# Performance work log

Measured on AMD Instinct MI355X. Metric: run time of the kernel, lower is better.

Reference implementation:

```python
import jax, jax.numpy as jnp
import numpy as np

NODE_DIM = 256
OUT_DIM = 512
NUM_HEADS = 8
HEAD_DIM = 32
HID = NUM_HEADS * HEAD_DIM  # 256
N_NODES = 200000
N_GRAPHS = 2000


def _linear_init(key, fan_in, fan_out):
    lim = 1.0 / np.sqrt(fan_in)
    kw, kb = jax.random.split(key)
    w = jax.random.uniform(kw, (fan_in, fan_out), minval=-lim, maxval=lim, dtype=jnp.float32)
    b = jax.random.uniform(kb, (fan_out,), minval=-lim, maxval=lim, dtype=jnp.float32)
    return w, b


def setup_inputs() -> dict:
    key = jax.random.key(0)
    ks = jax.random.split(key, 16)
    inp = {}
    inp["node_embeddings"] = jax.random.normal(ks[0], (N_NODES, NODE_DIM), dtype=jnp.float32)
    inp["node_to_graph_id"] = jnp.sort(jax.random.randint(ks[1], (N_NODES,), 0, N_GRAPHS)).astype(jnp.int64)
    inp["num_graphs"] = N_GRAPHS
    # weighted_mean pooler params
    inp["wm_score_w1"], inp["wm_score_b1"] = _linear_init(ks[2], NODE_DIM, HID)
    inp["wm_score_w2"], inp["wm_score_b2"] = _linear_init(ks[3], HID, NUM_HEADS)
    inp["wm_val_w1"], inp["wm_val_b1"] = _linear_init(ks[4], NODE_DIM, HID)
    inp["wm_val_w2"], inp["wm_val_b2"] = _linear_init(ks[5], HID, NUM_HEADS * HEAD_DIM)
    inp["wm_comb_w"] = _linear_init(ks[6], NUM_HEADS * HEAD_DIM, OUT_DIM)[0]
    # weighted_sum pooler params
    inp["ws_score_w1"], inp["ws_score_b1"] = _linear_init(ks[7], NODE_DIM, HID)
    inp["ws_score_w2"], inp["ws_score_b2"] = _linear_init(ks[8], HID, NUM_HEADS)
    inp["ws_val_w1"], inp["ws_val_b1"] = _linear_init(ks[9], NODE_DIM, HID)
    inp["ws_val_w2"], inp["ws_val_b2"] = _linear_init(ks[10], HID, NUM_HEADS * HEAD_DIM)
    inp["ws_comb_w"] = _linear_init(ks[11], NUM_HEADS * HEAD_DIM, OUT_DIM)[0]
    # max pooler + final combination
    inp["mx_comb_w"] = _linear_init(ks[12], NODE_DIM, OUT_DIM)[0]
    inp["final_w"] = _linear_init(ks[13], 3 * OUT_DIM, OUT_DIM)[0]
    return inp


def _mlp(x, w1, b1, w2, b2):
    return jax.nn.relu(x @ w1 + b1) @ w2 + b2


def _scatter_softmax(scores, seg, num_graphs):
    # scores: [N, H]; softmax over nodes within each graph, per head
    m = jax.ops.segment_max(scores, seg, num_segments=num_graphs)
    m = jnp.where(jnp.isfinite(m), m, 0.0)  # empty graphs
    e = jnp.exp(scores - m[seg])
    s = jax.ops.segment_sum(e, seg, num_segments=num_graphs)
    return e / s[seg]


def _multihead_readout(x, seg, num_graphs, sw1, sb1, sw2, sb2, vw1, vb1, vw2, vb2, cw, weighted_mean):
    scores = _mlp(x, sw1, sb1, sw2, sb2)                       # [N, heads]
    if weighted_mean:
        weights = _scatter_softmax(scores, seg, num_graphs)
    else:
        weights = jax.nn.sigmoid(scores)
    values = _mlp(x, vw1, vb1, vw2, vb2).reshape(-1, NUM_HEADS, HEAD_DIM)
    weighted = (weights[:, :, None] * values).reshape(-1, NUM_HEADS * HEAD_DIM)
    per_graph = jax.ops.segment_sum(weighted, seg, num_segments=num_graphs)
    return per_graph @ cw


def reference(node_embeddings, node_to_graph_id, num_graphs,
              wm_score_w1, wm_score_b1, wm_score_w2, wm_score_b2,
              wm_val_w1, wm_val_b1, wm_val_w2, wm_val_b2, wm_comb_w,
              ws_score_w1, ws_score_b1, ws_score_w2, ws_score_b2,
              ws_val_w1, ws_val_b1, ws_val_w2, ws_val_b2, ws_comb_w,
              mx_comb_w, final_w):
    seg = node_to_graph_id.astype(jnp.int32)
    mean_repr = _multihead_readout(node_embeddings, seg, num_graphs,
                                   wm_score_w1, wm_score_b1, wm_score_w2, wm_score_b2,
                                   wm_val_w1, wm_val_b1, wm_val_w2, wm_val_b2, wm_comb_w, True)
    sum_repr = _multihead_readout(node_embeddings, seg, num_graphs,
                                  ws_score_w1, ws_score_b1, ws_score_w2, ws_score_b2,
                                  ws_val_w1, ws_val_b1, ws_val_w2, ws_val_b2, ws_comb_w, False)
    pg_max = jax.ops.segment_max(node_embeddings, seg, num_segments=num_graphs)
    pg_max = jnp.where(jnp.isfinite(pg_max), pg_max, 0.0)  # torch_scatter zeros empty segments
    max_repr = pg_max @ mx_comb_w
    raw = jnp.concatenate([mean_repr, sum_repr, max_repr], axis=1)  # [G, 3*out_dim]
    return jax.nn.relu(raw) @ final_w
```

## Files before the change

### kernel.cpp

```cpp
#include <hip/hip_runtime.h>
#include <hip/hip_bf16.h>

typedef __bf16 bf16_t;
typedef __bf16 bf16x8 __attribute__((ext_vector_type(8)));
typedef float  f32x4  __attribute__((ext_vector_type(4)));

#define MFMA16(a, b, c) __builtin_amdgcn_mfma_f32_16x16x32_bf16((a), (b), (c), 0, 0, 0)

#define ROWS 48

__device__ __forceinline__ int gray(int row) { return (row ^ (row >> 1)) & 7; }
__device__ __forceinline__ int swz256(int row, int col) {
    return row * 256 + ((((col >> 3) ^ gray(row)) << 3) | (col & 7));
}

__device__ __forceinline__ bf16x8 cvt8(float4 a, float4 b) {
    bf16x8 o;
    o[0] = (bf16_t)a.x; o[1] = (bf16_t)a.y; o[2] = (bf16_t)a.z; o[3] = (bf16_t)a.w;
    o[4] = (bf16_t)b.x; o[5] = (bf16_t)b.y; o[6] = (bf16_t)b.z; o[7] = (bf16_t)b.w;
    return o;
}

__device__ __forceinline__ unsigned enc_max(float x) {
    unsigned b = __float_as_uint(x);
    return (b & 0x80000000u) ? ~b : (b | 0x80000000u);
}
__device__ __forceinline__ float dec_max(unsigned e) {
    if (e == 0u) return 0.0f;
    return (e & 0x80000000u) ? __uint_as_float(e ^ 0x80000000u) : __uint_as_float(~e);
}

__device__ __forceinline__ void gemm256p(const bf16_t* __restrict__ As,
                                         const bf16_t* __restrict__ Wk,
                                         f32x4 acc[3][2], int w, int l) {
    const int l15 = l & 15, hi = l >> 4;
#pragma unroll
    for (int mt = 0; mt < 3; ++mt)
#pragma unroll
        for (int j = 0; j < 2; ++j) acc[mt][j] = (f32x4){0.f, 0.f, 0.f, 0.f};

    const bf16_t* wb = Wk + ((size_t)hi * 256 + w * 32 + l15) * 8;

    bf16x8 b0[3], b1[3];
    bf16x8 a[2][3];
    b0[0] = *(const bf16x8*)(wb);
    b1[0] = *(const bf16x8*)(wb + 128);
    b0[1] = *(const bf16x8*)(wb + 8192);
    b1[1] = *(const bf16x8*)(wb + 8192 + 128);
#pragma unroll
    for (int mt = 0; mt < 3; ++mt) {
        const int row = mt * 16 + l15;
        a[0][mt] = *(const bf16x8*)(As + row * 256 + (hi ^ gray(row)) * 8);
    }

#pragma unroll
    for (int kt = 0; kt < 8; ++kt) {
        const int cur = kt % 3, nx2 = (kt + 2) % 3;
        if (kt + 2 < 8) {
            b0[nx2] = *(const bf16x8*)(wb + (kt + 2) * 8192);
            b1[nx2] = *(const bf16x8*)(wb + (kt + 2) * 8192 + 128);
        }
        if (kt + 1 < 8) {
#pragma unroll
            for (int mt = 0; mt < 3; ++mt) {
                const int row = mt * 16 + l15;
                a[(kt + 1) & 1][mt] =
                    *(const bf16x8*)(As + row * 256 + (((kt + 1) * 4 + hi) ^ gray(row)) * 8);
            }
        }
#pragma unroll
        for (int mt = 0; mt < 3; ++mt) {
            acc[mt][0] = MFMA16(a[kt & 1][mt], b0[cur], acc[mt][0]);
            acc[mt][1] = MFMA16(a[kt & 1][mt], b1[cur], acc[mt][1]);
        }
    }
}

__device__ __forceinline__ void write_h(f32x4 acc[3][2], const float* __restrict__ bias,
                                        bool relu, bf16_t* __restrict__ dst, int w, int l) {
    const int l15 = l & 15, hi = l >> 4;
#pragma unroll
    for (int j = 0; j < 2; ++j) {
        const int col = w * 32 + j * 16 + l15;
        const float bv = bias[col];
#pragma unroll
        for (int mt = 0; mt < 3; ++mt)
#pragma unroll
            for (int r = 0; r < 4; ++r) {
                const int row = mt * 16 + hi * 4 + r;
                float v = acc[mt][j][r] + bv;
                if (relu) v = fmaxf(v, 0.f);
                dst[swz256(row, col)] = (bf16_t)v;
            }
    }
}

__device__ __forceinline__ void gemm_score(const bf16_t* __restrict__ As,
                                           const bf16_t* __restrict__ W2k,
                                           const float* __restrict__ b2,
                                           float* __restrict__ ssc, int coloff, int w, int l) {
    if (w >= 3) return;
    const int l15 = l & 15, hi = l >> 4;
    const int row = w * 16 + l15;
    const bf16_t* wb = W2k + ((size_t)hi * 16 + l15) * 8;
    bf16x8 b[3];
    b[0] = *(const bf16x8*)(wb);
    b[1] = *(const bf16x8*)(wb + 512);
    f32x4 acc = (f32x4){0.f, 0.f, 0.f, 0.f};
#pragma unroll
    for (int kt = 0; kt < 8; ++kt) {
        const int cur = kt % 3, nx2 = (kt + 2) % 3;
        if (kt + 2 < 8) b[nx2] = *(const bf16x8*)(wb + (kt + 2) * 512);
        bf16x8 a = *(const bf16x8*)(As + row * 256 + ((kt * 4 + hi) ^ gray(row)) * 8);
        acc = MFMA16(a, b[cur], acc);
    }
    if (l15 < 8) {
        const float bv = b2[l15];
#pragma unroll
        for (int r = 0; r < 4; ++r) {
            const int orow = w * 16 + hi * 4 + r;
            ssc[orow * 16 + coloff + l15] = acc[r] + bv;
        }
    }
}

template <bool WM>
__device__ __forceinline__ void reduce_seg(const bf16_t* __restrict__ sh,
                                           const float* __restrict__ ssc,
                                           const bf16_t* __restrict__ sx,
                                           const int* __restrict__ sseg,
                                           float* __restrict__ num, float* __restrict__ den,
                                           unsigned* __restrict__ pmax, int G) {
    const int col = threadIdx.x & 255;
    const int rbeg = (threadIdx.x >> 8) * 24;
    float av = 0.f, ad = 0.f;
    unsigned am = 0u;
    int gcur = sseg[rbeg];
    for (int r = rbeg; r < rbeg + 24; ++r) {
        const int g = sseg[r];
        if (g != gcur) {
            if ((unsigned)gcur < (unsigned)G) {
                atomicAdd(&num[(size_t)gcur * 256 + col], av);
                if (WM) {
                    if (col < 8) atomicAdd(&den[(size_t)gcur * 8 + col], ad);
                    atomicMax(&pmax[(size_t)gcur * 256 + col], am);
                }
            }
            av = 0.f; ad = 0.f; am = 0u; gcur = g;
        }
        const int si = swz256(r, col);
        const float v = (float)sh[si];
        const float wgt = ssc[r * 16 + (WM ? 0 : 8) + (col >> 5)];
        av += wgt * v;
        if (WM) {
            if (col < 8) ad += ssc[r * 16 + col];
            am = max(am, enc_max((float)sx[si]));
        }
    }
    if ((unsigned)gcur < (unsigned)G) {
        atomicAdd(&num[(size_t)gcur * 256 + col], av);
        if (WM) {
            if (col < 8) atomicAdd(&den[(size_t)gcur * 8 + col], ad);
            atomicMax(&pmax[(size_t)gcur * 256 + col], am);
        }
    }
}

__global__ __launch_bounds__(512, 3) void node_kernel(
    const float* __restrict__ X, const int* __restrict__ seg,
    const bf16_t* __restrict__ wt_sw1_wm, const bf16_t* __restrict__ wt_sw2_wm,
    const bf16_t* __restrict__ wt_vw1_wm, const bf16_t* __restrict__ wt_vw2_wm,
    const bf16_t* __restrict__ wt_sw1_ws, const bf16_t* __restrict__ wt_sw2_ws,
    const bf16_t* __restrict__ wt_vw1_ws, const bf16_t* __restrict__ wt_vw2_ws,
    const float* __restrict__ b_sw1_wm, const float* __restrict__ b_sw2_wm,
    const float* __restrict__ b_vw1_wm, const float* __restrict__ b_vw2_wm,
    const float* __restrict__ b_sw1_ws, const float* __restrict__ b_sw2_ws,
    const float* __restrict__ b_vw1_ws, const float* __restrict__ b_vw2_ws,
    float* __restrict__ num_wm, float* __restrict__ den_wm,
    float* __restrict__ acc_ws, unsigned* __restrict__ pmax, int N, int G) {
    __shared__ __align__(16) bf16_t sx[ROWS * 256];
    __shared__ __align__(16) bf16_t sh[ROWS * 256];
    __shared__ float ssc[ROWS * 16];
    __shared__ int sseg[ROWS];

    const int tid = threadIdx.x;
    const int w = tid >> 6, l = tid & 63;
    const int r0 = blockIdx.x * ROWS;

#pragma unroll
    for (int i = 0; i < 3; ++i) {
        const int cid = tid + i * 512;
        const int row = cid >> 5, ch = cid & 31;
        bf16x8 o;
        if (r0 + row < N) {
            const float4* gp = (const float4*)(X + (size_t)(r0 + row) * 256 + ch * 8);
            o = cvt8(gp[0], gp[1]);
        } else {
            for (int j = 0; j < 8; ++j) o[j] = (bf16_t)0.f;
        }
        *(bf16x8*)(sx + row * 256 + (ch ^ gray(row)) * 8) = o;
    }
    if (tid < ROWS) sseg[tid] = (r0 + tid < N) ? seg[r0 + tid] : -1;
    __syncthreads();

    f32x4 acc[3][2];

    gemm256p(sx, wt_sw1_wm, acc, w, l);
    write_h(acc, b_sw1_wm, true, sh, w, l);
    __syncthreads();
    gemm_score(sh, wt_sw2_wm, b_sw2_wm, ssc, 0, w, l);
    __syncthreads();

    gemm256p(sx, wt_sw1_ws, acc, w, l);
    write_h(acc, b_sw1_ws, true, sh, w, l);
    __syncthreads();
    gemm_score(sh, wt_sw2_ws, b_sw2_ws, ssc, 8, w, l);
    __syncthreads();

#pragma unroll
    for (int i = 0; i < 2; ++i) {
        const int idx = tid + i * 512;
        if (idx < ROWS * 16) {
            const float v = ssc[idx];
            ssc[idx] = ((idx & 15) < 8) ? __expf(v) : 1.f / (1.f + __expf(-v));
        }
    }
    __syncthreads();

    gemm256p(sx, wt_vw1_wm, acc, w, l);
    write_h(acc, b_vw1_wm, true, sh, w, l);
    __syncthreads();
    gemm256p(sh, wt_vw2_wm, acc, w, l);
    __syncthreads();
    write_h(acc, b_vw2_wm, false, sh, w, l);
    __syncthreads();
    reduce_seg<true>(sh, ssc, sx, sseg, num_wm, den_wm, pmax, G);
    __syncthreads();

    gemm256p(sx, wt_vw1_ws, acc, w, l);
    write_h(acc, b_vw1_ws, true, sh, w, l);
    __syncthreads();
    gemm256p(sh, wt_vw2_ws, acc, w, l);
    __syncthreads();
    write_h(acc, b_vw2_ws, false, sx, w, l);
    __syncthreads();
    reduce_seg<false>(sx, ssc, sx, sseg, acc_ws, nullptr, nullptr, G);
}

__global__ __launch_bounds__(256, 2) void graph_kernel(
    const float* __restrict__ num_wm, const float* __restrict__ den_wm,
    const float* __restrict__ acc_ws, const unsigned* __restrict__ pmax,
    const bf16_t* __restrict__ wt_comb_wm, const bf16_t* __restrict__ wt_comb_ws,
    const bf16_t* __restrict__ wt_comb_mx, const bf16_t* __restrict__ wt_final,
    float* __restrict__ out, int G) {
    __shared__ __align__(16) bf16_t sa[16 * 256];
    __shared__ __align__(16) bf16_t sraw[16 * 1536];

    const int tid = threadIdx.x, w = tid >> 6, l = tid & 63;
    const int l15 = l & 15, hi = l >> 4;
    const int g0 = blockIdx.x * 16;

    for (int src = 0; src < 3; ++src) {
#pragma unroll
        for (int i = 0; i < 2; ++i) {
            const int cid = tid + i * 256;
            const int row = cid >> 5, ch = cid & 31;
            const int g = g0 + row;
            bf16x8 o;
            if (g < G) {
                if (src == 0) {
                    const float4* np = (const float4*)(num_wm + (size_t)g * 256 + ch * 8);
                    float4 v0 = np[0], v1 = np[1];
                    const float d = den_wm[(size_t)g * 8 + (ch >> 2)];
                    const float rd = (d > 0.f) ? 1.f / d : 0.f;
                    o[0] = (bf16_t)(v0.x * rd); o[1] = (bf16_t)(v0.y * rd);
                    o[2] = (bf16_t)(v0.z * rd); o[3] = (bf16_t)(v0.w * rd);
                    o[4] = (bf16_t)(v1.x * rd); o[5] = (bf16_t)(v1.y * rd);
                    o[6] = (bf16_t)(v1.z * rd); o[7] = (bf16_t)(v1.w * rd);
                } else if (src == 1) {
                    const float4* np = (const float4*)(acc_ws + (size_t)g * 256 + ch * 8);
                    o = cvt8(np[0], np[1]);
                } else {
                    const unsigned* mp = pmax + (size_t)g * 256 + ch * 8;
#pragma unroll
                    for (int j = 0; j < 8; ++j) o[j] = (bf16_t)dec_max(mp[j]);
                }
            } else {
                for (int j = 0; j < 8; ++j) o[j] = (bf16_t)0.f;
            }
            *(bf16x8*)(sa + row * 256 + (ch ^ gray(row)) * 8) = o;
        }
        __syncthreads();

        const bf16_t* Wt = (src == 0) ? wt_comb_wm : ((src == 1) ? wt_comb_ws : wt_comb_mx);
        bf16x8 a[8];
#pragma unroll
        for (int kt = 0; kt < 8; ++kt)
            a[kt] = *(const bf16x8*)(sa + l15 * 256 + ((kt * 4 + hi) ^ gray(l15)) * 8);
        f32x4 acc[8];
#pragma unroll
        for (int j = 0; j < 8; ++j) acc[j] = (f32x4){0.f, 0.f, 0.f, 0.f};
#pragma unroll
        for (int kt = 0; kt < 8; ++kt) {
            bf16x8 b[8];
#pragma unroll
            for (int j = 0; j < 8; ++j) {
                const int ncol = (w * 8 + j) * 16 + l15;
                b[j] = *(const bf16x8*)(Wt + ((size_t)(kt * 4 + hi) * 512 + ncol) * 8);
            }
#pragma unroll
            for (int j = 0; j < 8; ++j) acc[j] = MFMA16(a[kt], b[j], acc[j]);
        }
#pragma unroll
        for (int j = 0; j < 8; ++j) {
            const int col = src * 512 + (w * 8 + j) * 16 + l15;
#pragma unroll
            for (int r = 0; r < 4; ++r) {
                const int row = hi * 4 + r;
                const float v = fmaxf(acc[j][r], 0.f);
                sraw[row * 1536 + ((((col >> 3) ^ gray(row)) << 3) | (col & 7))] = (bf16_t)v;
            }
        }
        __syncthreads();
    }

    f32x4 facc[8];
#pragma unroll
    for (int j = 0; j < 8; ++j) facc[j] = (f32x4){0.f, 0.f, 0.f, 0.f};
    for (int kt = 0; kt < 48; ++kt) {
        bf16x8 a = *(const bf16x8*)(sraw + l15 * 1536 + ((kt * 4 + hi) ^ gray(l15)) * 8);
#pragma unroll
        for (int j = 0; j < 8; ++j) {
            const int ncol = (w * 8 + j) * 16 + l15;
            bf16x8 b = *(const bf16x8*)(wt_final + ((size_t)(kt * 4 + hi) * 512 + ncol) * 8);
            facc[j] = MFMA16(a, b, facc[j]);
        }
    }
#pragma unroll
    for (int j = 0; j < 8; ++j) {
        const int col = (w * 8 + j) * 16 + l15;
#pragma unroll
        for (int r = 0; r < 4; ++r) {
            const int row = hi * 4 + r;
            if (g0 + row < G) out[(size_t)(g0 + row) * 512 + col] = facc[j][r];
        }
    }
}

struct PrepTab {
    const float* src[12];
    bf16_t* dst[12];
    int K[12], Nn[12], Nout[12];
    int base[13];
};

__global__ void prep_all(PrepTab t) {
    const int idx = blockIdx.x * blockDim.x + threadIdx.x;
    if (idx >= t.base[12]) return;
    int i = 0;
#pragma unroll
    for (int s = 0; s < 12; ++s)
        if (idx >= t.base[s + 1]) i = s + 1;
    const int local = idx - t.base[i];
    const int j = local & 7;
    const int rest = local >> 3;
    const int n = rest % t.Nout[i];
    const int kc = rest / t.Nout[i];
    const int k = kc * 8 + j;
    const float v = (n < t.Nn[i]) ? t.src[i][(size_t)k * t.Nn[i] + n] : 0.f;
    t.dst[i][local] = (bf16_t)v;
}

extern "C" void kernel_launch(void* const* d_in, const int* in_sizes, int n_in,
                              void* d_out, int out_size, void* d_ws, size_t ws_size,
                              hipStream_t stream) {
    const float* X = (const float*)d_in[0];
    const int* seg = (const int*)d_in[1];
    const int N = in_sizes[1];
    const int G = out_size / 512;

    float* num_wm = (float*)d_ws;
    float* acc_ws = num_wm + (size_t)G * 256;
    float* den_wm = acc_ws + (size_t)G * 256;
    unsigned* pmax = (unsigned*)(den_wm + (size_t)G * 8);
    bf16_t* wt = (bf16_t*)(pmax + (size_t)G * 256);

    bf16_t* wt_sw1_wm = wt;
    bf16_t* wt_sw2_wm = wt_sw1_wm + 65536;
    bf16_t* wt_vw1_wm = wt_sw2_wm + 4096;
    bf16_t* wt_vw2_wm = wt_vw1_wm + 65536;
    bf16_t* wt_sw1_ws = wt_vw2_wm + 65536;
    bf16_t* wt_sw2_ws = wt_sw1_ws + 65536;
    bf16_t* wt_vw1_ws = wt_sw2_ws + 4096;
    bf16_t* wt_vw2_ws = wt_vw1_ws + 65536;
    bf16_t* wt_comb_wm = wt_vw2_ws + 65536;
    bf16_t* wt_comb_ws = wt_comb_wm + 131072;
    bf16_t* wt_comb_mx = wt_comb_ws + 131072;
    bf16_t* wt_final = wt_comb_mx + 131072;

    const size_t accum_bytes = ((size_t)G * 256 * 3 + (size_t)G * 8) * 4;
    hipMemsetAsync(d_ws, 0, accum_bytes, stream);

    struct TT { int srcIdx; bf16_t* dst; int K, Nn, Nout; };
    const TT tt[12] = {
        {3,  wt_sw1_wm, 256, 256, 256},  {5,  wt_sw2_wm, 256, 8,   16},
        {7,  wt_vw1_wm, 256, 256, 256},  {9,  wt_vw2_wm, 256, 256, 256},
        {12, wt_sw1_ws, 256, 256, 256},  {14, wt_sw2_ws, 256, 8,   16},
        {16, wt_vw1_ws, 256, 256, 256},  {18, wt_vw2_ws, 256, 256, 256},
        {11, wt_comb_wm, 256, 512, 512}, {20, wt_comb_ws, 256, 512, 512},
        {21, wt_comb_mx, 256, 512, 512}, {22, wt_final, 1536, 512, 512},
    };
    PrepTab pt;
    int base = 0;
    for (int i = 0; i < 12; ++i) {
        pt.src[i] = (const float*)d_in[tt[i].srcIdx];
        pt.dst[i] = tt[i].dst;
        pt.K[i] = tt[i].K; pt.Nn[i] = tt[i].Nn; pt.Nout[i] = tt[i].Nout;
        pt.base[i] = base;
        base += tt[i].K * tt[i].Nout;
    }
    pt.base[12] = base;
    prep_all<<<(base + 255) / 256, 256, 0, stream>>>(pt);

    const int nb = (N + ROWS - 1) / ROWS;
    node_kernel<<<nb, 512, 0, stream>>>(
        X, seg,
        wt_sw1_wm, wt_sw2_wm, wt_vw1_wm, wt_vw2_wm,
        wt_sw1_ws, wt_sw2_ws, wt_vw1_ws, wt_vw2_ws,
        (const float*)d_in[4], (const float*)d_in[6], (const float*)d_in[8], (const float*)d_in[10],
        (const float*)d_in[13], (const float*)d_in[15], (const float*)d_in[17], (const float*)d_in[19],
        num_wm, den_wm, acc_ws, pmax, N, G);

    const int gb = (G + 15) / 16;
    graph_kernel<<<gb, 256, 0, stream>>>(num_wm, den_wm, acc_ws, pmax,
                                         wt_comb_wm, wt_comb_ws, wt_comb_mx, wt_final,
                                         (float*)d_out, G);
}
```

Baseline: 302.9 us.

## Vectorize segment reductions and split sum/max work across thread halves

Replaces the per-column scalar segment reduction with an 8-wide bf16x8 vectorized version, where each thread owns 8 columns over 6 rows. The weighted-sum and max reductions now run concurrently on separate halves of the block instead of one thread doing both. The denominator is accumulated with one atomic per row and head rather than per segment run. This is meant to cut LDS load instructions and serial loop length in the reduction phase, at the cost of more global atomics, since runs are split over 6-row chunks, and idle threads in the second reduction.

```diff
diff --git a/kernel.cpp b/kernel.cpp
--- a/kernel.cpp
+++ b/kernel.cpp
@@ -125,44 +125,70 @@
 }
 
 template <bool WM>
-__device__ __forceinline__ void reduce_seg(const bf16_t* __restrict__ sh,
-                                           const float* __restrict__ ssc,
-                                           const bf16_t* __restrict__ sx,
-                                           const int* __restrict__ sseg,
-                                           float* __restrict__ num, float* __restrict__ den,
-                                           unsigned* __restrict__ pmax, int G) {
-    const int col = threadIdx.x & 255;
-    const int rbeg = (threadIdx.x >> 8) * 24;
-    float av = 0.f, ad = 0.f;
-    unsigned am = 0u;
+__device__ __forceinline__ void reduce_sum_vec(const bf16_t* __restrict__ sh,
+                                               const float* __restrict__ ssc,
+                                               const int* __restrict__ sseg,
+                                               float* __restrict__ num, int G, int tid) {
+    const int cg = tid & 31;
+    const int rbeg = (tid >> 5) * 6;
+    const int off = (WM ? 0 : 8) + (cg >> 2);
+    float s[8];
+#pragma unroll
+    for (int j = 0; j < 8; ++j) s[j] = 0.f;
     int gcur = sseg[rbeg];
-    for (int r = rbeg; r < rbeg + 24; ++r) {
+    for (int r = rbeg; r < rbeg + 6; ++r) {
         const int g = sseg[r];
         if (g != gcur) {
             if ((unsigned)gcur < (unsigned)G) {
-                atomicAdd(&num[(size_t)gcur * 256 + col], av);
-                if (WM) {
-                    if (col < 8) atomicAdd(&den[(size_t)gcur * 8 + col], ad);
-                    atomicMax(&pmax[(size_t)gcur * 256 + col], am);
-                }
-            }
-            av = 0.f; ad = 0.f; am = 0u; gcur = g;
-        }
-        const int si = swz256(r, col);
-        const float v = (float)sh[si];
-        const float wgt = ssc[r * 16 + (WM ? 0 : 8) + (col >> 5)];
-        av += wgt * v;
-        if (WM) {
-            if (col < 8) ad += ssc[r * 16 + col];
-            am = max(am, enc_max((float)sx[si]));
-        }
+#pragma unroll
+                for (int j = 0; j < 8; ++j)
+                    atomicAdd(&num[(size_t)gcur * 256 + cg * 8 + j], s[j]);
+            }
+#pragma unroll
+            for (int j = 0; j < 8; ++j) s[j] = 0.f;
+            gcur = g;
+        }
+        const float wgt = ssc[r * 16 + off];
+        const bf16x8 v = *(const bf16x8*)(sh + r * 256 + (cg ^ gray(r)) * 8);
+#pragma unroll
+        for (int j = 0; j < 8; ++j) s[j] += wgt * (float)v[j];
     }
     if ((unsigned)gcur < (unsigned)G) {
-        atomicAdd(&num[(size_t)gcur * 256 + col], av);
-        if (WM) {
-            if (col < 8) atomicAdd(&den[(size_t)gcur * 8 + col], ad);
-            atomicMax(&pmax[(size_t)gcur * 256 + col], am);
-        }
+#pragma unroll
+        for (int j = 0; j < 8; ++j)
+            atomicAdd(&num[(size_t)gcur * 256 + cg * 8 + j], s[j]);
+    }
+}
+
+__device__ __forceinline__ void max_vec(const bf16_t* __restrict__ sx,
+                                        const int* __restrict__ sseg,
+                                        unsigned* __restrict__ pmax, int G, int tid2) {
+    const int cg = tid2 & 31;
+    const int rbeg = (tid2 >> 5) * 6;
+    unsigned am[8];
+#pragma unroll
+    for (int j = 0; j < 8; ++j) am[j] = 0u;
+    int gcur = sseg[rbeg];
+    for (int r = rbeg; r < rbeg + 6; ++r) {
+        const int g = sseg[r];
+        if (g != gcur) {
+            if ((unsigned)gcur < (unsigned)G) {
+#pragma unroll
+                for (int j = 0; j < 8; ++j)
+                    atomicMax(&pmax[(size_t)gcur * 256 + cg * 8 + j], am[j]);
+            }
+#pragma unroll
+            for (int j = 0; j < 8; ++j) am[j] = 0u;
+            gcur = g;
+        }
+        const bf16x8 v = *(const bf16x8*)(sx + r * 256 + (cg ^ gray(r)) * 8);
+#pragma unroll
+        for (int j = 0; j < 8; ++j) am[j] = max(am[j], enc_max((float)v[j]));
+    }
+    if ((unsigned)gcur < (unsigned)G) {
+#pragma unroll
+        for (int j = 0; j < 8; ++j)
+            atomicMax(&pmax[(size_t)gcur * 256 + cg * 8 + j], am[j]);
     }
 }
 
@@ -234,7 +260,16 @@
     __syncthreads();
     write_h(acc, b_vw2_wm, false, sh, w, l);
     __syncthreads();
-    reduce_seg<true>(sh, ssc, sx, sseg, num_wm, den_wm, pmax, G);
+    if (tid < 256)
+        reduce_sum_vec<true>(sh, ssc, sseg, num_wm, G, tid);
+    else
+        max_vec(sx, sseg, pmax, G, tid - 256);
+    if (tid < ROWS * 8) {
+        const int row = tid >> 3, h = tid & 7;
+        const int g = sseg[row];
+        if ((unsigned)g < (unsigned)G)
+            atomicAdd(&den_wm[(size_t)g * 8 + h], ssc[row * 16 + h]);
+    }
     __syncthreads();
 
     gemm256p(sx, wt_vw1_ws, acc, w, l);
@@ -244,7 +279,8 @@
     __syncthreads();
     write_h(acc, b_vw2_ws, false, sx, w, l);
     __syncthreads();
-    reduce_seg<false>(sx, ssc, sx, sseg, acc_ws, nullptr, nullptr, G);
+    if (tid < 256)
+        reduce_sum_vec<false>(sx, ssc, sseg, acc_ws, G, tid);
 }
 
 __global__ __launch_bounds__(256, 2) void graph_kernel(
```

New measurement: 957.3 us. 3.16x slower.

## Pair the two poolers' first-layer GEMMs to share A-tile loads and cut barriers

Applied to the files above, without the earlier changes.

Adds a paired GEMM that computes the weighted-mean and weighted-sum first-layer projections together, so each A fragment read from shared memory feeds both weight sets. The two score heads now run at the same time on different wave groups. A second hidden buffer keeps both intermediate activations resident, which lets several barriers go. The launch bound is raised from 3 to 4 blocks per CU. The cost is more shared memory per block (an extra 24KB) and double the accumulator registers in the paired GEMM, so the higher occupancy target may not be met or may force register spills.

```diff
diff --git a/kernel.cpp b/kernel.cpp
--- a/kernel.cpp
+++ b/kernel.cpp
@@ -28,6 +28,58 @@
 __device__ __forceinline__ float dec_max(unsigned e) {
     if (e == 0u) return 0.0f;
     return (e & 0x80000000u) ? __uint_as_float(e ^ 0x80000000u) : __uint_as_float(~e);
+}
+
+__device__ __forceinline__ void gemm256_pair(const bf16_t* __restrict__ As,
+                                             const bf16_t* __restrict__ WkA,
+                                             const bf16_t* __restrict__ WkB,
+                                             f32x4 accA[3][2], f32x4 accB[3][2],
+                                             int w, int l) {
+    const int l15 = l & 15, hi = l >> 4;
+#pragma unroll
+    for (int mt = 0; mt < 3; ++mt)
+#pragma unroll
+        for (int j = 0; j < 2; ++j) {
+            accA[mt][j] = (f32x4){0.f, 0.f, 0.f, 0.f};
+            accB[mt][j] = (f32x4){0.f, 0.f, 0.f, 0.f};
+        }
+    const bf16_t* wbA = WkA + ((size_t)hi * 256 + w * 32 + l15) * 8;
+    const bf16_t* wbB = WkB + ((size_t)hi * 256 + w * 32 + l15) * 8;
+
+    bf16x8 bA0[2], bA1[2], bB0[2], bB1[2];
+    bf16x8 a[2][3];
+    bA0[0] = *(const bf16x8*)(wbA);
+    bA1[0] = *(const bf16x8*)(wbA + 128);
+    bB0[0] = *(const bf16x8*)(wbB);
+    bB1[0] = *(const bf16x8*)(wbB + 128);
+#pragma unroll
+    for (int mt = 0; mt < 3; ++mt) {
+        const int row = mt * 16 + l15;
+        a[0][mt] = *(const bf16x8*)(As + row * 256 + (hi ^ gray(row)) * 8);
+    }
+#pragma unroll
+    for (int kt = 0; kt < 8; ++kt) {
+        const int cur = kt & 1, nxt = cur ^ 1;
+        if (kt + 1 < 8) {
+            bA0[nxt] = *(const bf16x8*)(wbA + (kt + 1) * 8192);
+            bA1[nxt] = *(const bf16x8*)(wbA + (kt + 1) * 8192 + 128);
+            bB0[nxt] = *(const bf16x8*)(wbB + (kt + 1) * 8192);
+            bB1[nxt] = *(const bf16x8*)(wbB + (kt + 1) * 8192 + 128);
+#pragma unroll
+            for (int mt = 0; mt < 3; ++mt) {
+                const int row = mt * 16 + l15;
+                a[nxt][mt] =
+                    *(const bf16x8*)(As + row * 256 + (((kt + 1) * 4 + hi) ^ gray(row)) * 8);
+            }
+        }
+#pragma unroll
+        for (int mt = 0; mt < 3; ++mt) {
+            accA[mt][0] = MFMA16(a[cur][mt], bA0[cur], accA[mt][0]);
+            accA[mt][1] = MFMA16(a[cur][mt], bA1[cur], accA[mt][1]);
+            accB[mt][0] = MFMA16(a[cur][mt], bB0[cur], accB[mt][0]);
+            accB[mt][1] = MFMA16(a[cur][mt], bB1[cur], accB[mt][1]);
+        }
+    }
 }
 
 __device__ __forceinline__ void gemm256p(const bf16_t* __restrict__ As,
@@ -98,10 +150,9 @@
 __device__ __forceinline__ void gemm_score(const bf16_t* __restrict__ As,
                                            const bf16_t* __restrict__ W2k,
                                            const float* __restrict__ b2,
-                                           float* __restrict__ ssc, int coloff, int w, int l) {
-    if (w >= 3) return;
+                                           float* __restrict__ ssc, int coloff, int rt, int l) {
     const int l15 = l & 15, hi = l >> 4;
-    const int row = w * 16 + l15;
+    const int row = rt * 16 + l15;
     const bf16_t* wb = W2k + ((size_t)hi * 16 + l15) * 8;
     bf16x8 b[3];
     b[0] = *(const bf16x8*)(wb);
@@ -118,7 +169,7 @@
         const float bv = b2[l15];
 #pragma unroll
         for (int r = 0; r < 4; ++r) {
-            const int orow = w * 16 + hi * 4 + r;
+            const int orow = rt * 16 + hi * 4 + r;
             ssc[orow * 16 + coloff + l15] = acc[r] + bv;
         }
     }
@@ -166,7 +217,7 @@
     }
 }
 
-__global__ __launch_bounds__(512, 3) void node_kernel(
+__global__ __launch_bounds__(512, 4) void node_kernel(
     const float* __restrict__ X, const int* __restrict__ seg,
     const bf16_t* __restrict__ wt_sw1_wm, const bf16_t* __restrict__ wt_sw2_wm,
     const bf16_t* __restrict__ wt_vw1_wm, const bf16_t* __restrict__ wt_vw2_wm,
@@ -179,7 +230,8 @@
     float* __restrict__ num_wm, float* __restrict__ den_wm,
     float* __restrict__ acc_ws, unsigned* __restrict__ pmax, int N, int G) {
     __shared__ __align__(16) bf16_t sx[ROWS * 256];
-    __shared__ __align__(16) bf16_t sh[ROWS * 256];
+    __shared__ __align__(16) bf16_t shm[ROWS * 256];
+    __shared__ __align__(16) bf16_t shs[ROWS * 256];
     __shared__ float ssc[ROWS * 16];
     __shared__ int sseg[ROWS];
 
@@ -203,18 +255,17 @@
     if (tid < ROWS) sseg[tid] = (r0 + tid < N) ? seg[r0 + tid] : -1;
     __syncthreads();
 
-    f32x4 acc[3][2];
-
-    gemm256p(sx, wt_sw1_wm, acc, w, l);
-    write_h(acc, b_sw1_wm, true, sh, w, l);
-    __syncthreads();
-    gemm_score(sh, wt_sw2_wm, b_sw2_wm, ssc, 0, w, l);
-    __syncthreads();
-
-    gemm256p(sx, wt_sw1_ws, acc, w, l);
-    write_h(acc, b_sw1_ws, true, sh, w, l);
-    __syncthreads();
-    gemm_score(sh, wt_sw2_ws, b_sw2_ws, ssc, 8, w, l);
+    f32x4 accA[3][2], accB[3][2];
+
+    gemm256_pair(sx, wt_sw1_wm, wt_sw1_ws, accA, accB, w, l);
+    write_h(accA, b_sw1_wm, true, shm, w, l);
+    write_h(accB, b_sw1_ws, true, shs, w, l);
+    __syncthreads();
+
+    if (w < 3)
+        gemm_score(shm, wt_sw2_wm, b_sw2_wm, ssc, 0, w, l);
+    else if (w >= 4 && w < 7)
+        gemm_score(shs, wt_sw2_ws, b_sw2_ws, ssc, 8, w - 4, l);
     __syncthreads();
 
 #pragma unroll
@@ -227,24 +278,22 @@
     }
     __syncthreads();
 
-    gemm256p(sx, wt_vw1_wm, acc, w, l);
-    write_h(acc, b_vw1_wm, true, sh, w, l);
-    __syncthreads();
-    gemm256p(sh, wt_vw2_wm, acc, w, l);
-    __syncthreads();
-    write_h(acc, b_vw2_wm, false, sh, w, l);
-    __syncthreads();
-    reduce_seg<true>(sh, ssc, sx, sseg, num_wm, den_wm, pmax, G);
-    __syncthreads();
-
-    gemm256p(sx, wt_vw1_ws, acc, w, l);
-    write_h(acc, b_vw1_ws, true, sh, w, l);
-    __syncthreads();
-    gemm256p(sh, wt_vw2_ws, acc, w, l);
-    __syncthreads();
-    write_h(acc, b_vw2_ws, false, sx, w, l);
-    __syncthreads();
-    reduce_seg<false>(sx, ssc, sx, sseg, acc_ws, nullptr, nullptr, G);
+    gemm256_pair(sx, wt_vw1_wm, wt_vw1_ws, accA, accB, w, l);
+    write_h(accA, b_vw1_wm, true, shm, w, l);
+    write_h(accB, b_vw1_ws, true, shs, w, l);
+    __syncthreads();
+
+    gemm256p(shm, wt_vw2_wm, accA, w, l);
+    __syncthreads();
+    write_h(accA, b_vw2_wm, false, shm, w, l);
+    __syncthreads();
+    reduce_seg<true>(shm, ssc, sx, sseg, num_wm, den_wm, pmax, G);
+
+    gemm256p(shs, wt_vw2_ws, accA, w, l);
+    __syncthreads();
+    write_h(accA, b_vw2_ws, false, shs, w, l);
+    __syncthreads();
+    reduce_seg<false>(shs, ssc, sx, sseg, acc_ws, nullptr, nullptr, G);
 }
 
 __global__ __launch_bounds__(256, 2) void graph_kernel(
```

Result: slower. 354.9 us (+17.2%).

## Split node kernel across two grid rows, one per pooler

Applied to the files above, without the earlier changes.

The node kernel now launches a 2D grid where blockIdx.y picks either the weighted-mean or the weighted-sum pooler. Each block computes only one score MLP and one value MLP, halving the serial per-block work and doubling the block count. The max-pool reduction moves to the weighted-sum half. The cost is that every block reloads and converts its 48-row X tile, doubling input reads from global memory, and shared score storage is halved.

```diff
diff --git a/kernel.cpp b/kernel.cpp
--- a/kernel.cpp
+++ b/kernel.cpp
@@ -98,7 +98,7 @@
 __device__ __forceinline__ void gemm_score(const bf16_t* __restrict__ As,
                                            const bf16_t* __restrict__ W2k,
                                            const float* __restrict__ b2,
-                                           float* __restrict__ ssc, int coloff, int w, int l) {
+                                           float* __restrict__ ssc, int w, int l) {
     if (w >= 3) return;
     const int l15 = l & 15, hi = l >> 4;
     const int row = w * 16 + l15;
@@ -119,7 +119,7 @@
 #pragma unroll
         for (int r = 0; r < 4; ++r) {
             const int orow = w * 16 + hi * 4 + r;
-            ssc[orow * 16 + coloff + l15] = acc[r] + bv;
+            ssc[orow * 8 + l15] = acc[r] + bv;
         }
     }
 }
@@ -143,6 +143,7 @@
                 atomicAdd(&num[(size_t)gcur * 256 + col], av);
                 if (WM) {
                     if (col < 8) atomicAdd(&den[(size_t)gcur * 8 + col], ad);
+                } else {
                     atomicMax(&pmax[(size_t)gcur * 256 + col], am);
                 }
             }
@@ -150,10 +151,11 @@
         }
         const int si = swz256(r, col);
         const float v = (float)sh[si];
-        const float wgt = ssc[r * 16 + (WM ? 0 : 8) + (col >> 5)];
+        const float wgt = ssc[r * 8 + (col >> 5)];
         av += wgt * v;
         if (WM) {
-            if (col < 8) ad += ssc[r * 16 + col];
+            if (col < 8) ad += ssc[r * 8 + col];
+        } else {
             am = max(am, enc_max((float)sx[si]));
         }
     }
@@ -161,6 +163,7 @@
         atomicAdd(&num[(size_t)gcur * 256 + col], av);
         if (WM) {
             if (col < 8) atomicAdd(&den[(size_t)gcur * 8 + col], ad);
+        } else {
             atomicMax(&pmax[(size_t)gcur * 256 + col], am);
         }
     }
@@ -180,12 +183,22 @@
     float* __restrict__ acc_ws, unsigned* __restrict__ pmax, int N, int G) {
     __shared__ __align__(16) bf16_t sx[ROWS * 256];
     __shared__ __align__(16) bf16_t sh[ROWS * 256];
-    __shared__ float ssc[ROWS * 16];
+    __shared__ float ssc[ROWS * 8];
     __shared__ int sseg[ROWS];
 
     const int tid = threadIdx.x;
     const int w = tid >> 6, l = tid & 63;
     const int r0 = blockIdx.x * ROWS;
+    const bool wm = (blockIdx.y == 0);
+
+    const bf16_t* Ws1 = wm ? wt_sw1_wm : wt_sw1_ws;
+    const bf16_t* Ws2 = wm ? wt_sw2_wm : wt_sw2_ws;
+    const bf16_t* Wv1 = wm ? wt_vw1_wm : wt_vw1_ws;
+    const bf16_t* Wv2 = wm ? wt_vw2_wm : wt_vw2_ws;
+    const float* bs1 = wm ? b_sw1_wm : b_sw1_ws;
+    const float* bs2 = wm ? b_sw2_wm : b_sw2_ws;
+    const float* bv1 = wm ? b_vw1_wm : b_vw1_ws;
+    const float* bv2 = wm ? b_vw2_wm : b_vw2_ws;
 
 #pragma unroll
     for (int i = 0; i < 3; ++i) {
@@ -205,46 +218,30 @@
 
     f32x4 acc[3][2];
 
-    gemm256p(sx, wt_sw1_wm, acc, w, l);
-    write_h(acc, b_sw1_wm, true, sh, w, l);
-    __syncthreads();
-    gemm_score(sh, wt_sw2_wm, b_sw2_wm, ssc, 0, w, l);
-    __syncthreads();
-
-    gemm256p(sx, wt_sw1_ws, acc, w, l);
-    write_h(acc, b_sw1_ws, true, sh, w, l);
-    __syncthreads();
-    gemm_score(sh, wt_sw2_ws, b_sw2_ws, ssc, 8, w, l);
-    __syncthreads();
-
-#pragma unroll
-    for (int i = 0; i < 2; ++i) {
-        const int idx = tid + i * 512;
-        if (idx < ROWS * 16) {
-            const float v = ssc[idx];
-            ssc[idx] = ((idx & 15) < 8) ? __expf(v) : 1.f / (1.f + __expf(-v));
-        }
-    }
-    __syncthreads();
-
-    gemm256p(sx, wt_vw1_wm, acc, w, l);
-    write_h(acc, b_vw1_wm, true, sh, w, l);
-    __syncthreads();
-    gemm256p(sh, wt_vw2_wm, acc, w, l);
-    __syncthreads();
-    write_h(acc, b_vw2_wm, false, sh, w, l);
-    __syncthreads();
-    reduce_seg<true>(sh, ssc, sx, sseg, num_wm, den_wm, pmax, G);
-    __syncthreads();
-
-    gemm256p(sx, wt_vw1_ws, acc, w, l);
-    write_h(acc, b_vw1_ws, true, sh, w, l);
-    __syncthreads();
-    gemm256p(sh, wt_vw2_ws, acc, w, l);
-    __syncthreads();
-    write_h(acc, b_vw2_ws, false, sx, w, l);
-    __syncthreads();
-    reduce_seg<false>(sx, ssc, sx, sseg, acc_ws, nullptr, nullptr, G);
+    gemm256p(sx, Ws1, acc, w, l);
+    write_h(acc, bs1, true, sh, w, l);
+    __syncthreads();
+    gemm_score(sh, Ws2, bs2, ssc, w, l);
+    __syncthreads();
+
+    if (tid < ROWS * 8) {
+        const float v = ssc[tid];
+        ssc[tid] = wm ? __expf(v) : 1.f / (1.f + __expf(-v));
+    }
+    __syncthreads();
+
+    gemm256p(sx, Wv1, acc, w, l);
+    write_h(acc, bv1, true, sh, w, l);
+    __syncthreads();
+    gemm256p(sh, Wv2, acc, w, l);
+    __syncthreads();
+    write_h(acc, bv2, false, sh, w, l);
+    __syncthreads();
+
+    if (wm)
+        reduce_seg<true>(sh, ssc, sx, sseg, num_wm, den_wm, nullptr, G);
+    else
+        reduce_seg<false>(sh, ssc, sx, sseg, acc_ws, nullptr, pmax, G);
 }
 
 __global__ __launch_bounds__(256, 2) void graph_kernel(
@@ -423,7 +420,8 @@
     prep_all<<<(base + 255) / 256, 256, 0, stream>>>(pt);
 
     const int nb = (N + ROWS - 1) / ROWS;
-    node_kernel<<<nb, 512, 0, stream>>>(
+    dim3 ngrid(nb, 2);
+    node_kernel<<<ngrid, 512, 0, stream>>>(
         X, seg,
         wt_sw1_wm, wt_sw2_wm, wt_vw1_wm, wt_vw2_wm,
         wt_sw1_ws, wt_sw2_ws, wt_vw1_ws, wt_vw2_ws,
```

New measurement: 317.9 us. 1.05x slower.
